# Kernel tuning notes

Measured on AMD Instinct MI355X. Metric: run time of the kernel, lower is better.

Reference implementation:

```python
import jax, jax.numpy as jnp
import numpy as np

DIM = 1024
HEADS = 16
DIM_HEAD = 64
INNER = HEADS * DIM_HEAD
EPS = 1e-5


def layernorm(x, g, b):
    mu = jnp.mean(x, axis=-1, keepdims=True)
    var = jnp.var(x, axis=-1, keepdims=True)
    return (x - mu) * jax.lax.rsqrt(var + EPS) * g + b


def setup_inputs() -> dict:
    key = jax.random.key(0)
    ks = jax.random.split(key, 16)
    b, n = 2, 2048
    s = 0.02
    inp = {
        "x": jax.random.normal(ks[0], (b, n, DIM), dtype=jnp.float32),
        "ln_g": jnp.ones((DIM,), jnp.float32),
        "ln_b": jnp.zeros((DIM,), jnp.float32),
        "Wq": jax.random.normal(ks[1], (DIM, INNER), jnp.float32) * s,
        "Wkv": jax.random.normal(ks[2], (DIM, 2 * DIM_HEAD), jnp.float32) * s,
        "null_kv": jax.random.normal(ks[3], (2, DIM_HEAD), jnp.float32),
        "null_attn_bias": jax.random.normal(ks[4], (HEADS,), jnp.float32),
        "pb_w0": jax.random.normal(ks[5], (1, DIM), jnp.float32) * s,
        "pb_b0": jnp.zeros((DIM,), jnp.float32),
        "pb_ln0_g": jnp.ones((DIM,), jnp.float32),
        "pb_ln0_b": jnp.zeros((DIM,), jnp.float32),
        "pb_w1": jax.random.normal(ks[6], (DIM, DIM), jnp.float32) * s,
        "pb_b1": jnp.zeros((DIM,), jnp.float32),
        "pb_ln1_g": jnp.ones((DIM,), jnp.float32),
        "pb_ln1_b": jnp.zeros((DIM,), jnp.float32),
        "pb_w2": jax.random.normal(ks[7], (DIM, HEADS), jnp.float32) * s,
        "pb_b2": jnp.zeros((HEADS,), jnp.float32),
        "Wo": jax.random.normal(ks[8], (INNER, DIM), jnp.float32) * s,
        "out_ln_g": jnp.ones((DIM,), jnp.float32),
        "out_ln_b": jnp.zeros((DIM,), jnp.float32),
    }
    return inp


def dynamic_pos_bias(n, pb_w0, pb_b0, pb_ln0_g, pb_ln0_b, pb_w1, pb_b1,
                     pb_ln1_g, pb_ln1_b, pb_w2, pb_b2):
    # pos in [-(n-1), n-1], shape [2n-1, 1]
    pos = jnp.arange(-n + 1, n, dtype=jnp.float32)[:, None]
    h = jax.nn.silu(layernorm(pos @ pb_w0 + pb_b0, pb_ln0_g, pb_ln0_b))
    h = jax.nn.silu(layernorm(h @ pb_w1 + pb_b1, pb_ln1_g, pb_ln1_b))
    h = h @ pb_w2 + pb_b2  # [2n-1, heads]
    i = jnp.arange(n)
    idx = i[:, None] - i[None, :] + (n - 1)  # [n, n]
    bias = h[idx]  # [n, n, heads]
    return jnp.transpose(bias, (2, 0, 1))  # [heads, n, n]


def attention_fwd(x, ln_g, ln_b, Wq, Wkv, null_kv, null_attn_bias,
                  pb_w0, pb_b0, pb_ln0_g, pb_ln0_b, pb_w1, pb_b1,
                  pb_ln1_g, pb_ln1_b, pb_w2, pb_b2, Wo, out_ln_g, out_ln_b):
    b, n, _ = x.shape
    scale = DIM_HEAD ** -0.5
    xn = layernorm(x, ln_g, ln_b)
    q = (xn @ Wq).reshape(b, n, HEADS, DIM_HEAD).transpose(0, 2, 1, 3) * scale  # [b,h,n,d]
    kv = xn @ Wkv  # [b,n,2d]
    k, v = kv[..., :DIM_HEAD], kv[..., DIM_HEAD:]  # single-head MQA kv
    nk = jnp.broadcast_to(null_kv[0], (b, 1, DIM_HEAD))
    nv = jnp.broadcast_to(null_kv[1], (b, 1, DIM_HEAD))
    k = jnp.concatenate([nk, k], axis=1)  # [b, n+1, d]
    v = jnp.concatenate([nv, v], axis=1)
    sim = jnp.einsum('bhid,bjd->bhij', q, k)  # [b,h,n,n+1]
    rel = dynamic_pos_bias(n, pb_w0, pb_b0, pb_ln0_g, pb_ln0_b,
                           pb_w1, pb_b1, pb_ln1_g, pb_ln1_b, pb_w2, pb_b2)
    null_bias = jnp.broadcast_to(null_attn_bias[:, None, None], (HEADS, n, 1))
    attn_bias = jnp.concatenate([null_bias, rel], axis=-1)  # [h, n, n+1]
    sim = sim + attn_bias[None]
    max_neg = -jnp.finfo(sim.dtype).max
    causal_mask = jnp.triu(jnp.ones((n, n + 1), dtype=bool), k=2)
    sim = jnp.where(causal_mask[None, None], max_neg, sim)
    attn = jax.nn.softmax(sim, axis=-1)
    out = jnp.einsum('bhij,bjd->bhid', attn, v)  # [b,h,n,d]
    out = out.transpose(0, 2, 1, 3).reshape(b, n, INNER)
    return layernorm(out @ Wo, out_ln_g, out_ln_b)


def reference(x, ln_g, ln_b, Wq, Wkv, null_kv, null_attn_bias,
              pb_w0, pb_b0, pb_ln0_g, pb_ln0_b, pb_w1, pb_b1,
              pb_ln1_g, pb_ln1_b, pb_w2, pb_b2, Wo, out_ln_g, out_ln_b):
    return attention_fwd(x, ln_g, ln_b, Wq, Wkv, null_kv, null_attn_bias,
                         pb_w0, pb_b0, pb_ln0_g, pb_ln0_b, pb_w1, pb_b1,
                         pb_ln1_g, pb_ln1_b, pb_w2, pb_b2, Wo, out_ln_g, out_ln_b)
```

## Files before the change

### kernel.cpp

```cpp
#include <hip/hip_runtime.h>
#include <hip/hip_bf16.h>
#include <math.h>

#define DIMM   1024
#define NHEADS 16
#define DHEAD  64
#define BATCH  2
#define SEQ    2048
#define NKEYS  (SEQ + 1)
#define NKROWS 2112
#define NKP    2112
#define PBROWS (2 * SEQ - 1)
#define ROWS   (BATCH * SEQ)

using bf16x8 = __attribute__((ext_vector_type(8))) short;
using bf16x4 = __attribute__((ext_vector_type(4))) short;
using f32x4  = __attribute__((ext_vector_type(4))) float;
typedef unsigned int u32;
typedef unsigned short u16;

__device__ __forceinline__ u16 f2bf(float f) {
  __hip_bfloat16 h = __float2bfloat16(f);
  return __builtin_bit_cast(u16, h);
}
__device__ __forceinline__ float bf2f(u16 u) {
  u32 x = ((u32)u) << 16;
  return __builtin_bit_cast(float, x);
}
__device__ __forceinline__ void gl_lds16(const void* g, void* l) {
  __builtin_amdgcn_global_load_lds(
      (const __attribute__((address_space(1))) u32*)g,
      (__attribute__((address_space(3))) u32*)l, 16, 0, 0);
}
__device__ __forceinline__ f32x4 mfma16(bf16x4 a, bf16x4 b, f32x4 c) {
  asm("v_mfma_f32_16x16x16_bf16 %0, %1, %2, %0" : "+v"(c) : "v"(a), "v"(b));
  return c;
}

__global__ __launch_bounds__(256) void ln_kernel(
    const float* __restrict__ in, const float* __restrict__ addb,
    const float* __restrict__ g, const float* __restrict__ bvec,
    void* __restrict__ outv, int silu, int obf16, int posrow) {
  int row = blockIdx.x;
  int t = threadIdx.x;
  float4 x;
  if (posrow) {
    float p = (float)(row - (SEQ - 1));
    float4 wv = ((const float4*)in)[t];
    float4 a = ((const float4*)addb)[t];
    x.x = p * wv.x + a.x; x.y = p * wv.y + a.y;
    x.z = p * wv.z + a.z; x.w = p * wv.w + a.w;
  } else {
    x = ((const float4*)(in + (size_t)row * DIMM))[t];
    if (addb) {
      float4 a = ((const float4*)addb)[t];
      x.x += a.x; x.y += a.y; x.z += a.z; x.w += a.w;
    }
  }
  float s  = x.x + x.y + x.z + x.w;
  float ss = x.x * x.x + x.y * x.y + x.z * x.z + x.w * x.w;
#pragma unroll
  for (int off = 32; off > 0; off >>= 1) {
    s  += __shfl_down(s, off);
    ss += __shfl_down(ss, off);
  }
  __shared__ float rs[4], rss[4];
  int wv_ = t >> 6, lane = t & 63;
  if (lane == 0) { rs[wv_] = s; rss[wv_] = ss; }
  __syncthreads();
  float S  = rs[0] + rs[1] + rs[2] + rs[3];
  float SS = rss[0] + rss[1] + rss[2] + rss[3];
  float mu  = S * (1.0f / DIMM);
  float var = SS * (1.0f / DIMM) - mu * mu;
  float inv = rsqrtf(var + 1e-5f);
  float4 gv = ((const float4*)g)[t];
  float4 bv = ((const float4*)bvec)[t];
  float4 o;
  o.x = (x.x - mu) * inv * gv.x + bv.x;
  o.y = (x.y - mu) * inv * gv.y + bv.y;
  o.z = (x.z - mu) * inv * gv.z + bv.z;
  o.w = (x.w - mu) * inv * gv.w + bv.w;
  if (silu) {
    o.x = o.x / (1.f + expf(-o.x));
    o.y = o.y / (1.f + expf(-o.y));
    o.z = o.z / (1.f + expf(-o.z));
    o.w = o.w / (1.f + expf(-o.w));
  }
  if (obf16) {
    ushort4 ob;
    ob.x = f2bf(o.x); ob.y = f2bf(o.y); ob.z = f2bf(o.z); ob.w = f2bf(o.w);
    ((ushort4*)((u16*)outv + (size_t)row * DIMM))[t] = ob;
  } else {
    ((float4*)((float*)outv + (size_t)row * DIMM))[t] = o;
  }
}

__global__ __launch_bounds__(256) void conv_wT(
    const float* __restrict__ W, u16* __restrict__ WT, int N, int rowOff) {
  __shared__ float tile[32][33];
  const int n0 = blockIdx.x * 32, k0 = blockIdx.y * 32;
  const int tc = threadIdx.x & 31, tr = threadIdx.x >> 5;
#pragma unroll
  for (int i = 0; i < 4; ++i)
    tile[tr + i * 8][tc] = W[(size_t)(k0 + tr + i * 8) * N + n0 + tc];
  __syncthreads();
#pragma unroll
  for (int i = 0; i < 4; ++i) {
    int r = tr + i * 8;
    WT[(size_t)(rowOff + n0 + r) * 1024 + k0 + tc] = f2bf(tile[tc][r]);
  }
}

__global__ __launch_bounds__(256) void gemm_bf16(
    const u16* __restrict__ A, const u16* __restrict__ BT,
    float* __restrict__ C, int M, int N, int K) {
  __shared__ u16 As[128 * 32];
  __shared__ u16 Bs[128 * 32];
  const int w = threadIdx.x >> 6, lane = threadIdx.x & 63;
  const int lo = lane & 15, hi = lane >> 4;
  const int wr = w >> 1, wc = w & 1;
  const int row0 = blockIdx.y * 128, col0 = blockIdx.x * 128;
  const int srow = lane >> 2;
  const int scol = (lane & 3) * 8;
  f32x4 acc[4][4];
#pragma unroll
  for (int m = 0; m < 4; ++m)
#pragma unroll
    for (int n = 0; n < 4; ++n) acc[m][n] = f32x4{0.f, 0.f, 0.f, 0.f};
  for (int k0 = 0; k0 < K; k0 += 32) {
#pragma unroll
    for (int c = 0; c < 2; ++c) {
      const int base = 32 * w + c * 16;
      gl_lds16(A + (size_t)(row0 + base + srow) * K + k0 + scol,
               &As[base * 32]);
      gl_lds16(BT + (size_t)(col0 + base + srow) * K + k0 + scol,
               &Bs[base * 32]);
    }
    __syncthreads();
    bf16x8 af[4], bg[4];
#pragma unroll
    for (int m = 0; m < 4; ++m)
      af[m] = *(const bf16x8*)&As[(wr * 64 + m * 16 + lo) * 32 + hi * 8];
#pragma unroll
    for (int n = 0; n < 4; ++n)
      bg[n] = *(const bf16x8*)&Bs[(wc * 64 + n * 16 + lo) * 32 + hi * 8];
#pragma unroll
    for (int m = 0; m < 4; ++m)
#pragma unroll
      for (int n = 0; n < 4; ++n)
        acc[m][n] = __builtin_amdgcn_mfma_f32_16x16x32_bf16(af[m], bg[n],
                                                            acc[m][n], 0, 0, 0);
    __syncthreads();
  }
#pragma unroll
  for (int m = 0; m < 4; ++m)
#pragma unroll
    for (int r = 0; r < 4; ++r) {
      const int row = row0 + wr * 64 + m * 16 + hi * 4 + r;
      if (row < M) {
#pragma unroll
        for (int n = 0; n < 4; ++n)
          C[(size_t)row * N + col0 + wc * 64 + n * 16 + lo] = acc[m][n][r];
      }
    }
}

__global__ __launch_bounds__(256) void relayout_q(
    const float* __restrict__ tmp, u16* __restrict__ qb) {
  size_t e = (size_t)blockIdx.x * 256 + threadIdx.x;
  int m = (int)(e >> 8), c4 = (int)(e & 255);
  int b = m >> 11, i = m & 2047;
  int h = c4 >> 4, d4 = c4 & 15;
  float4 v = ((const float4*)(tmp + (size_t)m * 1152))[c4];
  const float sc = 0.125f;
  ushort4 o;
  o.x = f2bf(v.x * sc); o.y = f2bf(v.y * sc);
  o.z = f2bf(v.z * sc); o.w = f2bf(v.w * sc);
  ((ushort4*)qb)[((size_t)(b * NHEADS + h) * SEQ + i) * 16 + d4] = o;
}

__global__ __launch_bounds__(256) void relayout_kv(
    const float* __restrict__ tmp, u16* __restrict__ kb, u16* __restrict__ vbT) {
  size_t e = (size_t)blockIdx.x * 256 + threadIdx.x;
  int m = (int)(e >> 5), c4 = (int)(e & 31);
  int b = m >> 11, i = m & 2047;
  float4 v = ((const float4*)(tmp + (size_t)m * 1152 + 1024))[c4];
  if (c4 < 16) {
    ushort4 o;
    o.x = f2bf(v.x); o.y = f2bf(v.y); o.z = f2bf(v.z); o.w = f2bf(v.w);
    ((ushort4*)kb)[((size_t)b * NKROWS + (i + 1)) * 16 + c4] = o;
  } else {
    int d = (c4 - 16) * 4;
    size_t base = (size_t)b * DHEAD * NKP + (size_t)d * NKP + (i + 1);
    vbT[base]           = f2bf(v.x);
    vbT[base + NKP]     = f2bf(v.y);
    vbT[base + 2 * NKP] = f2bf(v.z);
    vbT[base + 3 * NKP] = f2bf(v.w);
  }
}

__global__ void fill_null(const float* __restrict__ null_kv,
                          u16* __restrict__ kb, u16* __restrict__ vbT) {
  int b = blockIdx.x, d = threadIdx.x;
  kb[(size_t)b * NKROWS * DHEAD + d] = f2bf(null_kv[d]);
  vbT[(size_t)b * DHEAD * NKP + (size_t)d * NKP] = f2bf(null_kv[DHEAD + d]);
}

__global__ __launch_bounds__(256) void h2_kernel(
    const u16* __restrict__ h1, const float* __restrict__ w2,
    const float* __restrict__ b2, float* __restrict__ bias_tabT) {
  int r = blockIdx.x, t = threadIdx.x;
  int col = t & 15, seg = t >> 4;
  const u16* hr = h1 + (size_t)r * DIMM;
  float acc = 0.f;
  for (int k = seg * 64; k < seg * 64 + 64; ++k)
    acc += bf2f(hr[k]) * w2[(size_t)k * NHEADS + col];
  __shared__ float p[16][16];
  p[seg][col] = acc;
  __syncthreads();
  if (t < 16) {
    float s = 0.f;
#pragma unroll
    for (int q = 0; q < 16; q++) s += p[q][t];
    bias_tabT[(size_t)t * 4096 + r] = s + b2[t];
  }
}

__global__ __launch_bounds__(128, 2) void flash_attn(
    const u16* __restrict__ qb, const u16* __restrict__ kb,
    const u16* __restrict__ vbT, const float* __restrict__ bias_tabT,
    const float* __restrict__ null_bias, u16* __restrict__ outb) {
  const int qt = gridDim.x - 1 - blockIdx.x;
  const int h = blockIdx.y, b = blockIdx.z;
  const int tid = threadIdx.x;
  const int w = tid >> 6, lane = tid & 63;
  const int lo = lane & 15, hi = lane >> 4;
  const int q0 = qt * 64;
  const int rq0 = q0 + w * 32 + lo;
  const int rq1 = rq0 + 16;

  __shared__ float bias_lds[2][128];

  const size_t qbase = (size_t)(b * NHEADS + h) * SEQ;
  const u16* qrow0 = qb + (qbase + rq0) * DHEAD;
  const u16* qrow1 = qb + (qbase + rq1) * DHEAD;
  bf16x8 qa00 = *(const bf16x8*)(qrow0 + hi * 8);
  bf16x8 qa01 = *(const bf16x8*)(qrow0 + 32 + hi * 8);
  bf16x8 qa10 = *(const bf16x8*)(qrow1 + hi * 8);
  bf16x8 qa11 = *(const bf16x8*)(qrow1 + 32 + hi * 8);

  const u16* Kb = kb + (size_t)b * NKROWS * DHEAD;
  const u16* Vb = vbT + (size_t)b * DHEAD * NKP;
  const float* bt = bias_tabT + (size_t)h * 4096;
  const float nb = null_bias[h];

  f32x4 o[2][4];
#pragma unroll
  for (int f = 0; f < 2; ++f)
#pragma unroll
    for (int dc = 0; dc < 4; ++dc) o[f][dc] = f32x4{0.f, 0.f, 0.f, 0.f};
  float m_l[2] = {-3.0e38f, -3.0e38f};
  float l_l[2] = {0.f, 0.f};

  const int nkt = qt + 2;
  bf16x8 kf0[4], kf1[4];
#pragma unroll
  for (int nf = 0; nf < 4; ++nf) {
    const u16* krow = Kb + (size_t)(nf * 16 + lo) * DHEAD;
    kf0[nf] = *(const bf16x8*)(krow + hi * 8);
    kf1[nf] = *(const bf16x8*)(krow + 32 + hi * 8);
  }

  for (int kt = 0; kt < nkt; ++kt) {
    const int j0 = kt * 64;
    {
      const int base = q0 - j0 - 63 + SEQ;
      if (tid < 127) bias_lds[kt & 1][tid] = bt[base + tid];
    }
    __syncthreads();
    f32x4 s[2][4];
    __builtin_amdgcn_s_setprio(1);
#pragma unroll
    for (int nf = 0; nf < 4; ++nf) {
      f32x4 a0 = f32x4{0.f, 0.f, 0.f, 0.f};
      f32x4 a1 = f32x4{0.f, 0.f, 0.f, 0.f};
      a0 = __builtin_amdgcn_mfma_f32_16x16x32_bf16(kf0[nf], qa00, a0, 0, 0, 0);
      a0 = __builtin_amdgcn_mfma_f32_16x16x32_bf16(kf1[nf], qa01, a0, 0, 0, 0);
      a1 = __builtin_amdgcn_mfma_f32_16x16x32_bf16(kf0[nf], qa10, a1, 0, 0, 0);
      a1 = __builtin_amdgcn_mfma_f32_16x16x32_bf16(kf1[nf], qa11, a1, 0, 0, 0);
      s[0][nf] = a0;
      s[1][nf] = a1;
    }
    __builtin_amdgcn_s_setprio(0);
    {
      const int jn = (kt + 1 < nkt ? kt + 1 : kt) * 64;
#pragma unroll
      for (int nf = 0; nf < 4; ++nf) {
        const u16* krow = Kb + (size_t)(jn + nf * 16 + lo) * DHEAD;
        kf0[nf] = *(const bf16x8*)(krow + hi * 8);
        kf1[nf] = *(const bf16x8*)(krow + 32 + hi * 8);
      }
    }
    bf16x4 vf[4][4];
#pragma unroll
    for (int dc = 0; dc < 4; ++dc) {
      const u16* vrow = Vb + (size_t)(dc * 16 + lo) * NKP + j0 + hi * 4;
#pragma unroll
      for (int kc = 0; kc < 4; ++kc)
        vf[dc][kc] = *(const bf16x4*)(vrow + kc * 16);
    }
    const float* bl = bias_lds[kt & 1];
    float tm[2] = {-3.0e38f, -3.0e38f};
#pragma unroll
    for (int f = 0; f < 2; ++f) {
      const int rq = (f == 0) ? rq0 : rq1;
      const int qrel = w * 32 + f * 16 + lo + 63;
#pragma unroll
      for (int nf = 0; nf < 4; ++nf)
#pragma unroll
        for (int r = 0; r < 4; ++r) {
          const int krel = nf * 16 + hi * 4 + r;
          const int key = j0 + krel;
          float bias = bl[qrel - krel];
          if (key == 0) bias = nb;
          float v = (key <= rq + 1) ? (s[f][nf][r] + bias) : -3.0e38f;
          s[f][nf][r] = v;
          tm[f] = fmaxf(tm[f], v);
        }
      tm[f] = fmaxf(tm[f], __shfl_xor(tm[f], 16));
      tm[f] = fmaxf(tm[f], __shfl_xor(tm[f], 32));
    }
    if (__any((tm[0] > m_l[0] + 8.0f) || (tm[1] > m_l[1] + 8.0f))) {
#pragma unroll
      for (int f = 0; f < 2; ++f) {
        float mn = fmaxf(m_l[f], tm[f]);
        float sco = __expf(m_l[f] - mn);
        m_l[f] = mn;
        l_l[f] *= sco;
#pragma unroll
        for (int dc = 0; dc < 4; ++dc)
#pragma unroll
          for (int r = 0; r < 4; ++r) o[f][dc][r] *= sco;
      }
    }
    bf16x4 pbf[2][4];
#pragma unroll
    for (int f = 0; f < 2; ++f)
#pragma unroll
      for (int nf = 0; nf < 4; ++nf) {
        float p0 = __expf(s[f][nf][0] - m_l[f]);
        float p1 = __expf(s[f][nf][1] - m_l[f]);
        float p2 = __expf(s[f][nf][2] - m_l[f]);
        float p3 = __expf(s[f][nf][3] - m_l[f]);
        l_l[f] += (p0 + p1) + (p2 + p3);
        pbf[f][nf][0] = (short)f2bf(p0);
        pbf[f][nf][1] = (short)f2bf(p1);
        pbf[f][nf][2] = (short)f2bf(p2);
        pbf[f][nf][3] = (short)f2bf(p3);
      }
    __builtin_amdgcn_s_setprio(1);
#pragma unroll
    for (int f = 0; f < 2; ++f)
#pragma unroll
      for (int dc = 0; dc < 4; ++dc)
#pragma unroll
        for (int kc = 0; kc < 4; ++kc)
          o[f][dc] = mfma16(vf[dc][kc], pbf[f][kc], o[f][dc]);
    __builtin_amdgcn_s_setprio(0);
  }
  asm volatile("s_nop 7\ns_nop 7" :::);
#pragma unroll
  for (int f = 0; f < 2; ++f) {
    float lf = l_l[f];
    lf += __shfl_xor(lf, 16);
    lf += __shfl_xor(lf, 32);
    float linv = 1.0f / lf;
    const int rq = (f == 0) ? rq0 : rq1;
    u16* orow = outb + (size_t)(b * SEQ + rq) * DIMM + h * DHEAD + hi * 4;
#pragma unroll
    for (int dc = 0; dc < 4; ++dc) {
      ushort4 st;
      st.x = f2bf(o[f][dc][0] * linv);
      st.y = f2bf(o[f][dc][1] * linv);
      st.z = f2bf(o[f][dc][2] * linv);
      st.w = f2bf(o[f][dc][3] * linv);
      *(ushort4*)(orow + dc * 16) = st;
    }
  }
}

extern "C" void kernel_launch(void* const* d_in, const int* in_sizes, int n_in,
                              void* d_out, int out_size, void* d_ws,
                              size_t ws_size, hipStream_t stream) {
  const float* x         = (const float*)d_in[0];
  const float* ln_g      = (const float*)d_in[1];
  const float* ln_b      = (const float*)d_in[2];
  const float* Wq        = (const float*)d_in[3];
  const float* Wkv       = (const float*)d_in[4];
  const float* null_kv   = (const float*)d_in[5];
  const float* null_bias = (const float*)d_in[6];
  const float* pb_w0     = (const float*)d_in[7];
  const float* pb_b0     = (const float*)d_in[8];
  const float* pb_ln0_g  = (const float*)d_in[9];
  const float* pb_ln0_b  = (const float*)d_in[10];
  const float* pb_w1     = (const float*)d_in[11];
  const float* pb_b1     = (const float*)d_in[12];
  const float* pb_ln1_g  = (const float*)d_in[13];
  const float* pb_ln1_b  = (const float*)d_in[14];
  const float* pb_w2     = (const float*)d_in[15];
  const float* pb_b2     = (const float*)d_in[16];
  const float* Wo        = (const float*)d_in[17];
  const float* out_ln_g  = (const float*)d_in[18];
  const float* out_ln_b  = (const float*)d_in[19];
  float* out = (float*)d_out;

  char* ws = (char*)d_ws;
  float* regA      = (float*)(ws);
  u16*   h1_bf     = (u16*)(ws + 18874368);
  u16*   regC      = (u16*)(ws + 35651584);
  u16*   qb        = (u16*)(ws + 44040192);
  u16*   kb        = (u16*)(ws + 52428800);
  u16*   vbT       = (u16*)(ws + 52969472);
  u16*   wqkvT     = (u16*)(ws + 53510144);
  u16*   w1T       = (u16*)(ws + 55869440);
  u16*   woT       = (u16*)(ws + 57966592);
  float* bias_tabT = (float*)(ws + 60063744);

  hipMemsetAsync((void*)kb, 0, 1081344, stream);

  conv_wT<<<dim3(32, 32), 256, 0, stream>>>(Wq, wqkvT, 1024, 0);
  conv_wT<<<dim3(4, 32), 256, 0, stream>>>(Wkv, wqkvT, 128, 1024);
  conv_wT<<<dim3(32, 32), 256, 0, stream>>>(pb_w1, w1T, 1024, 0);
  conv_wT<<<dim3(32, 32), 256, 0, stream>>>(Wo, woT, 1024, 0);

  ln_kernel<<<ROWS, 256, 0, stream>>>(x, nullptr, ln_g, ln_b, regC, 0, 1, 0);
  gemm_bf16<<<dim3(9, 32), 256, 0, stream>>>(regC, wqkvT, regA, ROWS, 1152,
                                             1024);
  relayout_q<<<4096, 256, 0, stream>>>(regA, qb);
  relayout_kv<<<512, 256, 0, stream>>>(regA, kb, vbT);
  fill_null<<<2, 64, 0, stream>>>(null_kv, kb, vbT);
  ln_kernel<<<PBROWS, 256, 0, stream>>>(pb_w0, pb_b0, pb_ln0_g, pb_ln0_b, regC,
                                        1, 1, 1);
  gemm_bf16<<<dim3(8, 32), 256, 0, stream>>>(regC, w1T, regA, PBROWS, 1024,
                                             1024);
  ln_kernel<<<PBROWS, 256, 0, stream>>>(regA, pb_b1, pb_ln1_g, pb_ln1_b, h1_bf,
                                        1, 1, 0);
  h2_kernel<<<PBROWS, 256, 0, stream>>>(h1_bf, pb_w2, pb_b2, bias_tabT);
  flash_attn<<<dim3(SEQ / 64, NHEADS, BATCH), 128, 0, stream>>>(
      qb, kb, vbT, bias_tabT, null_bias, regC);
  gemm_bf16<<<dim3(8, 32), 256, 0, stream>>>(regC, woT, regA, ROWS, 1024, 1024);
  ln_kernel<<<ROWS, 256, 0, stream>>>(regA, nullptr, out_ln_g, out_ln_b, out, 0,
                                      0, 0);
}
```

Measured before the change: 435.3 us.

## Split-K GEMMs with atomics, widen flash-attn key tile to 128, vectorize h2

All three GEMMs now split K across two z-blocks and accumulate into C with float atomicAdd, which needs a memset of the output beforehand. The goal is more blocks per launch on a GPU with many CUs. Flash attention now processes 128 keys per iteration instead of 64 and drops the register prefetch of the next K tile, so the key-row padding and bias LDS buffer grow to match. h2_kernel reads its activations as 8-wide vectors. Atomics and the extra memsets add memory traffic, and the larger attention tile raises register pressure at the cost of losing K prefetch.

After: 616.5 us. 41.6% more time.

```diff
diff --git a/kernel.cpp b/kernel.cpp
--- a/kernel.cpp
+++ b/kernel.cpp
@@ -8,8 +8,8 @@
 #define BATCH  2
 #define SEQ    2048
 #define NKEYS  (SEQ + 1)
-#define NKROWS 2112
-#define NKP    2112
+#define NKROWS 2176
+#define NKP    2176
 #define PBROWS (2 * SEQ - 1)
 #define ROWS   (BATCH * SEQ)
 
@@ -120,6 +120,7 @@
   const int lo = lane & 15, hi = lane >> 4;
   const int wr = w >> 1, wc = w & 1;
   const int row0 = blockIdx.y * 128, col0 = blockIdx.x * 128;
+  const int kz0 = blockIdx.z * (K >> 1), kz1 = kz0 + (K >> 1);
   const int srow = lane >> 2;
   const int scol = (lane & 3) * 8;
   f32x4 acc[4][4];
@@ -127,7 +128,7 @@
   for (int m = 0; m < 4; ++m)
 #pragma unroll
     for (int n = 0; n < 4; ++n) acc[m][n] = f32x4{0.f, 0.f, 0.f, 0.f};
-  for (int k0 = 0; k0 < K; k0 += 32) {
+  for (int k0 = kz0; k0 < kz1; k0 += 32) {
 #pragma unroll
     for (int c = 0; c < 2; ++c) {
       const int base = 32 * w + c * 16;
@@ -160,7 +161,8 @@
       if (row < M) {
 #pragma unroll
         for (int n = 0; n < 4; ++n)
-          C[(size_t)row * N + col0 + wc * 64 + n * 16 + lo] = acc[m][n][r];
+          atomicAdd(&C[(size_t)row * N + col0 + wc * 64 + n * 16 + lo],
+                    acc[m][n][r]);
       }
     }
 }
@@ -211,10 +213,16 @@
     const float* __restrict__ b2, float* __restrict__ bias_tabT) {
   int r = blockIdx.x, t = threadIdx.x;
   int col = t & 15, seg = t >> 4;
-  const u16* hr = h1 + (size_t)r * DIMM;
+  const u16* hr = h1 + (size_t)r * DIMM + seg * 64;
+  const float* w2s = w2 + (size_t)seg * 64 * NHEADS + col;
   float acc = 0.f;
-  for (int k = seg * 64; k < seg * 64 + 64; ++k)
-    acc += bf2f(hr[k]) * w2[(size_t)k * NHEADS + col];
+#pragma unroll
+  for (int c = 0; c < 8; ++c) {
+    bf16x8 hv = *(const bf16x8*)(hr + c * 8);
+#pragma unroll
+    for (int j = 0; j < 8; ++j)
+      acc += bf2f((u16)hv[j]) * w2s[(size_t)(c * 8 + j) * NHEADS];
+  }
   __shared__ float p[16][16];
   p[seg][col] = acc;
   __syncthreads();
@@ -239,7 +247,7 @@
   const int rq0 = q0 + w * 32 + lo;
   const int rq1 = rq0 + 16;
 
-  __shared__ float bias_lds[2][128];
+  __shared__ float bias_lds[2][192];
 
   const size_t qbase = (size_t)(b * NHEADS + h) * SEQ;
   const u16* qrow0 = qb + (qbase + rq0) * DHEAD;
@@ -262,51 +270,43 @@
   float m_l[2] = {-3.0e38f, -3.0e38f};
   float l_l[2] = {0.f, 0.f};
 
-  const int nkt = qt + 2;
-  bf16x8 kf0[4], kf1[4];
-#pragma unroll
-  for (int nf = 0; nf < 4; ++nf) {
-    const u16* krow = Kb + (size_t)(nf * 16 + lo) * DHEAD;
-    kf0[nf] = *(const bf16x8*)(krow + hi * 8);
-    kf1[nf] = *(const bf16x8*)(krow + 32 + hi * 8);
-  }
-
+  const int nkt = (qt + 3) >> 1;
   for (int kt = 0; kt < nkt; ++kt) {
-    const int j0 = kt * 64;
+    const int j0 = kt * 128;
     {
-      const int base = q0 - j0 - 63 + SEQ;
-      if (tid < 127) bias_lds[kt & 1][tid] = bt[base + tid];
+      const int base = q0 - j0 - 127 + SEQ;
+      float* blw = bias_lds[kt & 1];
+      blw[tid] = bt[base + tid];
+      if (tid < 63) blw[128 + tid] = bt[base + 128 + tid];
     }
     __syncthreads();
-    f32x4 s[2][4];
+    bf16x8 kfa[8], kfb[8];
+#pragma unroll
+    for (int nf = 0; nf < 8; ++nf) {
+      const u16* krow = Kb + (size_t)(j0 + nf * 16 + lo) * DHEAD;
+      kfa[nf] = *(const bf16x8*)(krow + hi * 8);
+      kfb[nf] = *(const bf16x8*)(krow + 32 + hi * 8);
+    }
+    f32x4 s[2][8];
     __builtin_amdgcn_s_setprio(1);
 #pragma unroll
-    for (int nf = 0; nf < 4; ++nf) {
+    for (int nf = 0; nf < 8; ++nf) {
       f32x4 a0 = f32x4{0.f, 0.f, 0.f, 0.f};
       f32x4 a1 = f32x4{0.f, 0.f, 0.f, 0.f};
-      a0 = __builtin_amdgcn_mfma_f32_16x16x32_bf16(kf0[nf], qa00, a0, 0, 0, 0);
-      a0 = __builtin_amdgcn_mfma_f32_16x16x32_bf16(kf1[nf], qa01, a0, 0, 0, 0);
-      a1 = __builtin_amdgcn_mfma_f32_16x16x32_bf16(kf0[nf], qa10, a1, 0, 0, 0);
-      a1 = __builtin_amdgcn_mfma_f32_16x16x32_bf16(kf1[nf], qa11, a1, 0, 0, 0);
+      a0 = __builtin_amdgcn_mfma_f32_16x16x32_bf16(kfa[nf], qa00, a0, 0, 0, 0);
+      a0 = __builtin_amdgcn_mfma_f32_16x16x32_bf16(kfb[nf], qa01, a0, 0, 0, 0);
+      a1 = __builtin_amdgcn_mfma_f32_16x16x32_bf16(kfa[nf], qa10, a1, 0, 0, 0);
+      a1 = __builtin_amdgcn_mfma_f32_16x16x32_bf16(kfb[nf], qa11, a1, 0, 0, 0);
       s[0][nf] = a0;
       s[1][nf] = a1;
     }
     __builtin_amdgcn_s_setprio(0);
-    {
-      const int jn = (kt + 1 < nkt ? kt + 1 : kt) * 64;
-#pragma unroll
-      for (int nf = 0; nf < 4; ++nf) {
-        const u16* krow = Kb + (size_t)(jn + nf * 16 + lo) * DHEAD;
-        kf0[nf] = *(const bf16x8*)(krow + hi * 8);
-        kf1[nf] = *(const bf16x8*)(krow + 32 + hi * 8);
-      }
-    }
-    bf16x4 vf[4][4];
+    bf16x4 vf[4][8];
 #pragma unroll
     for (int dc = 0; dc < 4; ++dc) {
       const u16* vrow = Vb + (size_t)(dc * 16 + lo) * NKP + j0 + hi * 4;
 #pragma unroll
-      for (int kc = 0; kc < 4; ++kc)
+      for (int kc = 0; kc < 8; ++kc)
         vf[dc][kc] = *(const bf16x4*)(vrow + kc * 16);
     }
     const float* bl = bias_lds[kt & 1];
@@ -314,14 +314,14 @@
 #pragma unroll
     for (int f = 0; f < 2; ++f) {
       const int rq = (f == 0) ? rq0 : rq1;
-      const int qrel = w * 32 + f * 16 + lo + 63;
-#pragma unroll
-      for (int nf = 0; nf < 4; ++nf)
+      const int qoff = w * 32 + f * 16 + lo + 127;
+#pragma unroll
+      for (int nf = 0; nf < 8; ++nf)
 #pragma unroll
         for (int r = 0; r < 4; ++r) {
           const int krel = nf * 16 + hi * 4 + r;
           const int key = j0 + krel;
-          float bias = bl[qrel - krel];
+          float bias = bl[qoff - krel];
           if (key == 0) bias = nb;
           float v = (key <= rq + 1) ? (s[f][nf][r] + bias) : -3.0e38f;
           s[f][nf][r] = v;
@@ -343,11 +343,11 @@
           for (int r = 0; r < 4; ++r) o[f][dc][r] *= sco;
       }
     }
-    bf16x4 pbf[2][4];
+    bf16x4 pbf[2][8];
 #pragma unroll
     for (int f = 0; f < 2; ++f)
 #pragma unroll
-      for (int nf = 0; nf < 4; ++nf) {
+      for (int nf = 0; nf < 8; ++nf) {
         float p0 = __expf(s[f][nf][0] - m_l[f]);
         float p1 = __expf(s[f][nf][1] - m_l[f]);
         float p2 = __expf(s[f][nf][2] - m_l[f]);
@@ -364,7 +364,7 @@
 #pragma unroll
       for (int dc = 0; dc < 4; ++dc)
 #pragma unroll
-        for (int kc = 0; kc < 4; ++kc)
+        for (int kc = 0; kc < 8; ++kc)
           o[f][dc] = mfma16(vf[dc][kc], pbf[f][kc], o[f][dc]);
     __builtin_amdgcn_s_setprio(0);
   }
@@ -420,13 +420,13 @@
   u16*   regC      = (u16*)(ws + 35651584);
   u16*   qb        = (u16*)(ws + 44040192);
   u16*   kb        = (u16*)(ws + 52428800);
-  u16*   vbT       = (u16*)(ws + 52969472);
-  u16*   wqkvT     = (u16*)(ws + 53510144);
-  u16*   w1T       = (u16*)(ws + 55869440);
-  u16*   woT       = (u16*)(ws + 57966592);
-  float* bias_tabT = (float*)(ws + 60063744);
-
-  hipMemsetAsync((void*)kb, 0, 1081344, stream);
+  u16*   vbT       = (u16*)(ws + 52985856);
+  u16*   wqkvT     = (u16*)(ws + 53542912);
+  u16*   w1T       = (u16*)(ws + 55902208);
+  u16*   woT       = (u16*)(ws + 57999360);
+  float* bias_tabT = (float*)(ws + 60096512);
+
+  hipMemsetAsync((void*)kb, 0, 1114112, stream);
 
   conv_wT<<<dim3(32, 32), 256, 0, stream>>>(Wq, wqkvT, 1024, 0);
   conv_wT<<<dim3(4, 32), 256, 0, stream>>>(Wkv, wqkvT, 128, 1024);
@@ -434,21 +434,25 @@
   conv_wT<<<dim3(32, 32), 256, 0, stream>>>(Wo, woT, 1024, 0);
 
   ln_kernel<<<ROWS, 256, 0, stream>>>(x, nullptr, ln_g, ln_b, regC, 0, 1, 0);
-  gemm_bf16<<<dim3(9, 32), 256, 0, stream>>>(regC, wqkvT, regA, ROWS, 1152,
-                                             1024);
+  hipMemsetAsync((void*)regA, 0, 18874368, stream);
+  gemm_bf16<<<dim3(9, 32, 2), 256, 0, stream>>>(regC, wqkvT, regA, ROWS, 1152,
+                                                1024);
   relayout_q<<<4096, 256, 0, stream>>>(regA, qb);
   relayout_kv<<<512, 256, 0, stream>>>(regA, kb, vbT);
   fill_null<<<2, 64, 0, stream>>>(null_kv, kb, vbT);
   ln_kernel<<<PBROWS, 256, 0, stream>>>(pb_w0, pb_b0, pb_ln0_g, pb_ln0_b, regC,
                                         1, 1, 1);
-  gemm_bf16<<<dim3(8, 32), 256, 0, stream>>>(regC, w1T, regA, PBROWS, 1024,
-                                             1024);
+  hipMemsetAsync((void*)regA, 0, 16773120, stream);
+  gemm_bf16<<<dim3(8, 32, 2), 256, 0, stream>>>(regC, w1T, regA, PBROWS, 1024,
+                                                1024);
   ln_kernel<<<PBROWS, 256, 0, stream>>>(regA, pb_b1, pb_ln1_g, pb_ln1_b, h1_bf,
                                         1, 1, 0);
   h2_kernel<<<PBROWS, 256, 0, stream>>>(h1_bf, pb_w2, pb_b2, bias_tabT);
   flash_attn<<<dim3(SEQ / 64, NHEADS, BATCH), 128, 0, stream>>>(
       qb, kb, vbT, bias_tabT, null_bias, regC);
-  gemm_bf16<<<dim3(8, 32), 256, 0, stream>>>(regC, woT, regA, ROWS, 1024, 1024);
+  hipMemsetAsync((void*)regA, 0, 16777216, stream);
+  gemm_bf16<<<dim3(8, 32, 2), 256, 0, stream>>>(regC, woT, regA, ROWS, 1024,
+                                                1024);
   ln_kernel<<<ROWS, 256, 0, stream>>>(regA, nullptr, out_ln_g, out_ln_b, out, 0,
                                       0, 0);
 }
```
